# Performance work log

Hardware: AMD Instinct MI355X
Metric: run time of the kernel (lower is better)

## Reference

```python
import jax, jax.numpy as jnp
import numpy as np

N = 500_000
MOL_C = 128
HID_C = 256
NUM_GRAPHS = 16384


def setup_inputs() -> dict:
    key = jax.random.key(0)
    ks = jax.random.split(key, 7)
    fan_lin = (MOL_C + HID_C) ** -0.5
    fan_last = HID_C ** -0.5
    return {
        "input_rep": jax.random.normal(ks[0], (N, MOL_C), dtype=jnp.float32),
        "final_rep": jax.random.normal(ks[1], (N, HID_C), dtype=jnp.float32),
        "graph_index": jnp.sort(jax.random.randint(ks[2], (N,), 0, NUM_GRAPHS, dtype=jnp.int32)),
        "W_lin": jax.random.normal(ks[3], (HID_C, MOL_C + HID_C), dtype=jnp.float32) * fan_lin,
        "b_lin": jax.random.normal(ks[4], (HID_C,), dtype=jnp.float32) * fan_lin,
        "W_last": jax.random.normal(ks[5], (HID_C, HID_C), dtype=jnp.float32) * fan_last,
        "b_last": jax.random.normal(ks[6], (HID_C,), dtype=jnp.float32) * fan_last,
    }


def reference(input_rep, final_rep, graph_index, W_lin, b_lin, W_last, b_last):
    # att = sigmoid(Linear(cat([input_rep, final_rep], dim=1)))  -> [N, HID_C]
    cat = jnp.concatenate([input_rep, final_rep], axis=1)
    att = jax.nn.sigmoid(cat @ W_lin.T + b_lin)
    # gated value: att * Linear(final_rep)  -> [N, HID_C]
    g = att * (final_rep @ W_last.T + b_last)
    # scatter_add over nodes -> [NUM_GRAPHS, HID_C]
    return jax.ops.segment_sum(g, graph_index, num_segments=NUM_GRAPHS)
```

## Files before the change

kernel.cpp:

```cpp
#include <hip/hip_runtime.h>
#include <hip/hip_bf16.h>


#define MOLC 128
#define HIDC 256
#define KTOT 384
#define NKT  12
#define TILE_N 64
#define NTHREADS 256

typedef _Float16 f16;
typedef _Float16 f16x8 __attribute__((ext_vector_type(8)));
typedef float    f32x4 __attribute__((ext_vector_type(4)));

__device__ __host__ __forceinline__ int swz(int r) { return (r ^ (r >> 2)) & 3; }

__device__ __forceinline__ f16x8 cvt8(float4 a, float4 b) {
  f16x8 r;
  r[0] = (f16)a.x; r[1] = (f16)a.y; r[2] = (f16)a.z; r[3] = (f16)a.w;
  r[4] = (f16)b.x; r[5] = (f16)b.y; r[6] = (f16)b.z; r[7] = (f16)b.w;
  return r;
}

#define GLL16(g, l) __builtin_amdgcn_global_load_lds(                          \
    (const __attribute__((address_space(1))) uint32_t*)(g),                    \
    (__attribute__((address_space(3))) uint32_t*)(l), 16, 0, 0)

__global__ void zero_out_kernel(float4* __restrict__ p, int n4) {
  int i = blockIdx.x * blockDim.x + threadIdx.x;
  if (i < n4) p[i] = make_float4(0.f, 0.f, 0.f, 0.f);
}

__global__ void pack_weights_kernel(const float* __restrict__ W_lin,
                                    const float* __restrict__ W_last,
                                    f16* __restrict__ ws) {
  int s = blockIdx.x * blockDim.x + threadIdx.x;
  if (s >= 20480) return;
  const float* src;
  f16* dst;
  if (s < 12288) {
    int ks = s >> 10, r = (s >> 2) & 255, c = s & 3;
    src = W_lin + (size_t)r * KTOT + ks * 32 + ((c ^ swz(r)) * 8);
    dst = ws + (size_t)s * 8;
  } else {
    int s2 = s - 12288;
    int ks = s2 >> 10, r = (s2 >> 2) & 255, c = s2 & 3;
    src = W_last + (size_t)r * HIDC + ks * 32 + ((c ^ swz(r)) * 8);
    dst = ws + 98304 + (size_t)s2 * 8;
  }
  f16x8 v;
#pragma unroll
  for (int j = 0; j < 8; ++j) v[j] = (f16)src[j];
  *(f16x8*)dst = v;
}

__device__ __forceinline__ void stage_w(const f16* gtile, f16* ltile, int wv, int lane) {
#pragma unroll
  for (int c = 0; c < 4; ++c) {
    const int off = (wv * 4 + c) * 1024 + lane * 16;
    GLL16((const char*)gtile + off, (char*)ltile + off);
  }
}

__global__ __launch_bounds__(NTHREADS, 2) void attn_pool_kernel(
    const float* __restrict__ input_rep,
    const float* __restrict__ final_rep,
    const int*   __restrict__ gidx,
    const f16*   __restrict__ ws,
    const float* __restrict__ b_lin,
    const float* __restrict__ b_last,
    float* __restrict__ out,
    int n_nodes)
{
  __shared__ f16 Abuf[2][TILE_N * 32];
  __shared__ f16 W1buf[2][HIDC * 32];
  __shared__ f16 W2buf[2][HIDC * 32];
  __shared__ int gi[TILE_N];

  const int t    = threadIdx.x;
  const int nb   = blockIdx.x * TILE_N;
  const int vn   = min(TILE_N, n_nodes - nb);
  const int lane = t & 63;
  const int wv   = t >> 6;
  const int wch  = wv * 64;
  const int lr   = lane & 15;
  const int lq   = lane >> 4;
  const int sl   = (lq ^ swz(lr)) * 8;

  const int arow  = t >> 2;
  const int aslot = t & 3;
  const int awslot = (aslot ^ swz(arow)) * 8;

  if (t < TILE_N) gi[t] = (nb + t < n_nodes) ? gidx[nb + t] : -1;

  const f16* wsW1 = ws;
  const f16* wsW2 = ws + 98304;

  stage_w(wsW1, W1buf[0], wv, lane);
  {
    float4 x0, x1;
    if (arow < vn) {
      const float* src = input_rep + (size_t)(nb + arow) * MOLC + aslot * 8;
      x0 = ((const float4*)src)[0];
      x1 = ((const float4*)src)[1];
    } else {
      x0 = make_float4(0.f, 0.f, 0.f, 0.f); x1 = x0;
    }
    *(f16x8*)&Abuf[0][arow * 32 + awslot] = cvt8(x0, x1);
  }
  __syncthreads();

  f32x4 acc1[4][4], acc2[4][4];
#pragma unroll
  for (int i = 0; i < 4; ++i)
#pragma unroll
    for (int j = 0; j < 4; ++j) { acc1[i][j] = (f32x4)(0.f); acc2[i][j] = (f32x4)(0.f); }

  for (int ks = 0; ks < NKT; ++ks) {
    const int cur = ks & 1, nxt = cur ^ 1;
    const int kn  = ks + 1;
    const bool pf = (kn < NKT);

    float4 x0, x1;
    if (pf) {
      stage_w(wsW1 + kn * 8192, W1buf[nxt], wv, lane);
      if (kn >= 4) stage_w(wsW2 + (kn - 4) * 8192, W2buf[nxt], wv, lane);
      if (arow < vn) {
        const float* src = (kn < 4)
            ? input_rep + (size_t)(nb + arow) * MOLC + kn * 32 + aslot * 8
            : final_rep + (size_t)(nb + arow) * HIDC + (kn * 32 - MOLC) + aslot * 8;
        x0 = ((const float4*)src)[0];
        x1 = ((const float4*)src)[1];
      } else {
        x0 = make_float4(0.f, 0.f, 0.f, 0.f); x1 = x0;
      }
    }

    f16x8 af[4];
#pragma unroll
    for (int i = 0; i < 4; ++i)
      af[i] = *(const f16x8*)&Abuf[cur][(i * 16 + lr) * 32 + sl];

    {
      f16x8 bf[4];
#pragma unroll
      for (int j = 0; j < 4; ++j)
        bf[j] = *(const f16x8*)&W1buf[cur][(wch + j * 16 + lr) * 32 + sl];
#pragma unroll
      for (int i = 0; i < 4; ++i)
#pragma unroll
        for (int j = 0; j < 4; ++j)
          acc1[i][j] = __builtin_amdgcn_mfma_f32_16x16x32_f16(af[i], bf[j], acc1[i][j], 0, 0, 0);
    }
    if (ks >= 4) {
      f16x8 bf[4];
#pragma unroll
      for (int j = 0; j < 4; ++j)
        bf[j] = *(const f16x8*)&W2buf[cur][(wch + j * 16 + lr) * 32 + sl];
#pragma unroll
      for (int i = 0; i < 4; ++i)
#pragma unroll
        for (int j = 0; j < 4; ++j)
          acc2[i][j] = __builtin_amdgcn_mfma_f32_16x16x32_f16(af[i], bf[j], acc2[i][j], 0, 0, 0);
    }

    if (pf) *(f16x8*)&Abuf[nxt][arow * 32 + awslot] = cvt8(x0, x1);

    __syncthreads();
  }

  float bl[4], bb[4];
#pragma unroll
  for (int j = 0; j < 4; ++j) {
    bl[j] = b_lin[wch + j * 16 + lr];
    bb[j] = b_last[wch + j * 16 + lr];
  }
#pragma unroll
  for (int i = 0; i < 4; ++i)
#pragma unroll
    for (int j = 0; j < 4; ++j)
#pragma unroll
      for (int r = 0; r < 4; ++r) {
        float a   = acc1[i][j][r] + bl[j];
        float att = 1.f / (1.f + __expf(-a));
        acc1[i][j][r] = att * (acc2[i][j][r] + bb[j]);
      }

  for (int i = 0; i < 4; ++i) {
    const int base = i * 16;
    int myg[4];
#pragma unroll
    for (int r = 0; r < 4; ++r) myg[r] = gi[base + lq * 4 + r];

    int s = 0;
    while (s < 16) {
      const int gid = gi[base + s];
      int e = s + 1;
      while (e < 16 && gi[base + e] == gid) ++e;
      if (gid >= 0) {
#pragma unroll
        for (int j = 0; j < 4; ++j) {
          float v = 0.f;
#pragma unroll
          for (int r = 0; r < 4; ++r)
            if (myg[r] == gid) v += acc1[i][j][r];
          v += __shfl_xor(v, 16);
          v += __shfl_xor(v, 32);
          if (lane < 16)
            atomicAdd(&out[(size_t)gid * HIDC + wch + j * 16 + lane], v);
        }
      }
      s = e;
    }
  }
}

extern "C" void kernel_launch(void* const* d_in, const int* in_sizes, int n_in,
                              void* d_out, int out_size, void* d_ws, size_t ws_size,
                              hipStream_t stream) {
  const float* input_rep = (const float*)d_in[0];
  const float* final_rep = (const float*)d_in[1];
  const int*   gidx      = (const int*)d_in[2];
  const float* W_lin     = (const float*)d_in[3];
  const float* b_lin     = (const float*)d_in[4];
  const float* W_last    = (const float*)d_in[5];
  const float* b_last    = (const float*)d_in[6];
  float* out = (float*)d_out;
  f16*   ws  = (f16*)d_ws;

  const int n_nodes = in_sizes[0] / MOLC;

  const int n4 = out_size / 4;
  zero_out_kernel<<<(n4 + 255) / 256, 256, 0, stream>>>((float4*)out, n4);

  pack_weights_kernel<<<80, 256, 0, stream>>>(W_lin, W_last, ws);

  const int grid = (n_nodes + TILE_N - 1) / TILE_N;
  attn_pool_kernel<<<grid, NTHREADS, 0, stream>>>(
      input_rep, final_rep, gidx, ws, b_lin, b_last, out, n_nodes);
}
```

Baseline: 1.022 ms.

## Load activations directly into MFMA registers, double tile with 8 waves, prepack weight fragments

The block tile grows to 128 nodes with 512 threads arranged as 2x4 waves, so each weight tile staged in LDS is reused by twice as many rows. Activation fragments are now loaded straight from global memory into registers in MFMA operand layout and converted to fp16 there, which removes the LDS staging buffer for A. Weights are prepacked in per-lane fragment order so the LDS reads need no swizzle. Synchronisation uses raw s_barrier with explicit vmcnt waits and scheduling barriers in place of __syncthreads. The per-lane activation loads are less coalesced and register pressure goes up.

```diff
diff --git a/kernel.cpp b/kernel.cpp
--- a/kernel.cpp
+++ b/kernel.cpp
@@ -6,14 +6,20 @@
 #define HIDC 256
 #define KTOT 384
 #define NKT  12
-#define TILE_N 64
-#define NTHREADS 256
+#define TILE_N 128
+#define NTH  512
 
 typedef _Float16 f16;
 typedef _Float16 f16x8 __attribute__((ext_vector_type(8)));
 typedef float    f32x4 __attribute__((ext_vector_type(4)));
 
-__device__ __host__ __forceinline__ int swz(int r) { return (r ^ (r >> 2)) & 3; }
+#define SBAR()  __builtin_amdgcn_s_barrier()
+#define SCHED() __builtin_amdgcn_sched_barrier(0)
+#define WAITV8() asm volatile("s_waitcnt vmcnt(8)" ::: "memory")
+
+#define GLL16(g, l) __builtin_amdgcn_global_load_lds(                          \
+    (const __attribute__((address_space(1))) uint32_t*)(g),                    \
+    (__attribute__((address_space(3))) uint32_t*)(l), 16, 0, 0)
 
 __device__ __forceinline__ f16x8 cvt8(float4 a, float4 b) {
   f16x8 r;
@@ -21,10 +27,6 @@
   r[4] = (f16)b.x; r[5] = (f16)b.y; r[6] = (f16)b.z; r[7] = (f16)b.w;
   return r;
 }
-
-#define GLL16(g, l) __builtin_amdgcn_global_load_lds(                          \
-    (const __attribute__((address_space(1))) uint32_t*)(g),                    \
-    (__attribute__((address_space(3))) uint32_t*)(l), 16, 0, 0)
 
 __global__ void zero_out_kernel(float4* __restrict__ p, int n4) {
   int i = blockIdx.x * blockDim.x + threadIdx.x;
@@ -39,30 +41,23 @@
   const float* src;
   f16* dst;
   if (s < 12288) {
-    int ks = s >> 10, r = (s >> 2) & 255, c = s & 3;
-    src = W_lin + (size_t)r * KTOT + ks * 32 + ((c ^ swz(r)) * 8);
+    int ks = s >> 10, rem = s & 1023, g = rem >> 6, lane = rem & 63;
+    int lr = lane & 15, lq = lane >> 4;
+    src = W_lin + (size_t)(g * 16 + lr) * KTOT + ks * 32 + lq * 8;
     dst = ws + (size_t)s * 8;
   } else {
     int s2 = s - 12288;
-    int ks = s2 >> 10, r = (s2 >> 2) & 255, c = s2 & 3;
-    src = W_last + (size_t)r * HIDC + ks * 32 + ((c ^ swz(r)) * 8);
+    int ks = s2 >> 10, rem = s2 & 1023, g = rem >> 6, lane = rem & 63;
+    int lr = lane & 15, lq = lane >> 4;
+    src = W_last + (size_t)(g * 16 + lr) * HIDC + ks * 32 + lq * 8;
     dst = ws + 98304 + (size_t)s2 * 8;
   }
-  f16x8 v;
-#pragma unroll
-  for (int j = 0; j < 8; ++j) v[j] = (f16)src[j];
-  *(f16x8*)dst = v;
-}
-
-__device__ __forceinline__ void stage_w(const f16* gtile, f16* ltile, int wv, int lane) {
-#pragma unroll
-  for (int c = 0; c < 4; ++c) {
-    const int off = (wv * 4 + c) * 1024 + lane * 16;
-    GLL16((const char*)gtile + off, (char*)ltile + off);
-  }
-}
-
-__global__ __launch_bounds__(NTHREADS, 2) void attn_pool_kernel(
+  float4 a = ((const float4*)src)[0];
+  float4 b = ((const float4*)src)[1];
+  *(f16x8*)dst = cvt8(a, b);
+}
+
+__global__ __launch_bounds__(NTH, 2) void attn_pool_kernel(
     const float* __restrict__ input_rep,
     const float* __restrict__ final_rep,
     const int*   __restrict__ gidx,
@@ -72,43 +67,53 @@
     float* __restrict__ out,
     int n_nodes)
 {
-  __shared__ f16 Abuf[2][TILE_N * 32];
-  __shared__ f16 W1buf[2][HIDC * 32];
-  __shared__ f16 W2buf[2][HIDC * 32];
+  __shared__ f16 W[2][16384];
   __shared__ int gi[TILE_N];
 
   const int t    = threadIdx.x;
-  const int nb   = blockIdx.x * TILE_N;
-  const int vn   = min(TILE_N, n_nodes - nb);
   const int lane = t & 63;
   const int wv   = t >> 6;
-  const int wch  = wv * 64;
+  const int wm   = wv >> 2;
+  const int wn   = wv & 3;
   const int lr   = lane & 15;
   const int lq   = lane >> 4;
-  const int sl   = (lq ^ swz(lr)) * 8;
-
-  const int arow  = t >> 2;
-  const int aslot = t & 3;
-  const int awslot = (aslot ^ swz(arow)) * 8;
+  const int nb   = blockIdx.x * TILE_N;
+  const int wch  = wn * 64;
 
   if (t < TILE_N) gi[t] = (nb + t < n_nodes) ? gidx[nb + t] : -1;
 
-  const f16* wsW1 = ws;
-  const f16* wsW2 = ws + 98304;
-
-  stage_w(wsW1, W1buf[0], wv, lane);
-  {
-    float4 x0, x1;
-    if (arow < vn) {
-      const float* src = input_rep + (size_t)(nb + arow) * MOLC + aslot * 8;
-      x0 = ((const float4*)src)[0];
-      x1 = ((const float4*)src)[1];
-    } else {
-      x0 = make_float4(0.f, 0.f, 0.f, 0.f); x1 = x0;
-    }
-    *(f16x8*)&Abuf[0][arow * 32 + awslot] = cvt8(x0, x1);
-  }
-  __syncthreads();
+  int offin[4], offfin[4];
+#pragma unroll
+  for (int i = 0; i < 4; ++i) {
+    int r = nb + wm * 64 + i * 16 + lr;
+    r = min(r, n_nodes - 1);
+    offin[i]  = r * MOLC;
+    offfin[i] = r * HIDC;
+  }
+
+  auto stageW1 = [&](int ks, int b) {
+#pragma unroll
+    for (int rd = 0; rd < 2; ++rd)
+      GLL16(ws + ks * 8192 + rd * 4096 + t * 8, &W[b][rd * 4096 + t * 8]);
+  };
+  auto stageW2 = [&](int ks, int b) {
+#pragma unroll
+    for (int rd = 0; rd < 2; ++rd)
+      GLL16(ws + 98304 + (ks - 4) * 8192 + rd * 4096 + t * 8,
+            &W[b][8192 + rd * 4096 + t * 8]);
+  };
+
+  float4 ra[4][2];
+  auto loadA = [&](int ks) {
+#pragma unroll
+    for (int i = 0; i < 4; ++i) {
+      const float* p = (ks < 4)
+          ? input_rep + offin[i]  + ks * 32 + lq * 8
+          : final_rep + offfin[i] + (ks - 4) * 32 + lq * 8;
+      ra[i][0] = ((const float4*)p)[0];
+      ra[i][1] = ((const float4*)p)[1];
+    }
+  };
 
   f32x4 acc1[4][4], acc2[4][4];
 #pragma unroll
@@ -116,36 +121,38 @@
 #pragma unroll
     for (int j = 0; j < 4; ++j) { acc1[i][j] = (f32x4)(0.f); acc2[i][j] = (f32x4)(0.f); }
 
+  stageW1(0, 0);
+  SCHED();
+  loadA(0);
+  SCHED();
+  asm volatile("s_waitcnt lgkmcnt(0)" ::: "memory");
+  WAITV8();
+  SCHED();
+  SBAR();
+
+#pragma unroll
   for (int ks = 0; ks < NKT; ++ks) {
-    const int cur = ks & 1, nxt = cur ^ 1;
-    const int kn  = ks + 1;
-    const bool pf = (kn < NKT);
-
-    float4 x0, x1;
-    if (pf) {
-      stage_w(wsW1 + kn * 8192, W1buf[nxt], wv, lane);
-      if (kn >= 4) stage_w(wsW2 + (kn - 4) * 8192, W2buf[nxt], wv, lane);
-      if (arow < vn) {
-        const float* src = (kn < 4)
-            ? input_rep + (size_t)(nb + arow) * MOLC + kn * 32 + aslot * 8
-            : final_rep + (size_t)(nb + arow) * HIDC + (kn * 32 - MOLC) + aslot * 8;
-        x0 = ((const float4*)src)[0];
-        x1 = ((const float4*)src)[1];
-      } else {
-        x0 = make_float4(0.f, 0.f, 0.f, 0.f); x1 = x0;
-      }
-    }
+    const int b = ks & 1, nx = b ^ 1;
+
+    if (ks + 1 < NKT) {
+      stageW1(ks + 1, nx);
+      if (ks + 1 >= 4) stageW2(ks + 1, nx);
+    }
+    SCHED();
 
     f16x8 af[4];
 #pragma unroll
-    for (int i = 0; i < 4; ++i)
-      af[i] = *(const f16x8*)&Abuf[cur][(i * 16 + lr) * 32 + sl];
+    for (int i = 0; i < 4; ++i) af[i] = cvt8(ra[i][0], ra[i][1]);
+    SCHED();
+
+    if (ks + 1 < NKT) loadA(ks + 1);
+    SCHED();
 
     {
       f16x8 bf[4];
 #pragma unroll
       for (int j = 0; j < 4; ++j)
-        bf[j] = *(const f16x8*)&W1buf[cur][(wch + j * 16 + lr) * 32 + sl];
+        bf[j] = *(const f16x8*)&W[b][(wn * 4 + j) * 512 + (lq * 16 + lr) * 8];
 #pragma unroll
       for (int i = 0; i < 4; ++i)
 #pragma unroll
@@ -156,7 +163,7 @@
       f16x8 bf[4];
 #pragma unroll
       for (int j = 0; j < 4; ++j)
-        bf[j] = *(const f16x8*)&W2buf[cur][(wch + j * 16 + lr) * 32 + sl];
+        bf[j] = *(const f16x8*)&W[b][8192 + (wn * 4 + j) * 512 + (lq * 16 + lr) * 8];
 #pragma unroll
       for (int i = 0; i < 4; ++i)
 #pragma unroll
@@ -164,9 +171,11 @@
           acc2[i][j] = __builtin_amdgcn_mfma_f32_16x16x32_f16(af[i], bf[j], acc2[i][j], 0, 0, 0);
     }
 
-    if (pf) *(f16x8*)&Abuf[nxt][arow * 32 + awslot] = cvt8(x0, x1);
-
-    __syncthreads();
+    if (ks + 1 < NKT) {
+      WAITV8();
+      SCHED();
+      SBAR();
+    }
   }
 
   float bl[4], bb[4];
@@ -187,7 +196,7 @@
       }
 
   for (int i = 0; i < 4; ++i) {
-    const int base = i * 16;
+    const int base = wm * 64 + i * 16;
     int myg[4];
 #pragma unroll
     for (int r = 0; r < 4; ++r) myg[r] = gi[base + lq * 4 + r];
@@ -236,6 +245,6 @@
   pack_weights_kernel<<<80, 256, 0, stream>>>(W_lin, W_last, ws);
 
   const int grid = (n_nodes + TILE_N - 1) / TILE_N;
-  attn_pool_kernel<<<grid, NTHREADS, 0, stream>>>(
+  attn_pool_kernel<<<grid, NTH, 0, stream>>>(
       input_rep, final_rep, gidx, ws, b_lin, b_last, out, n_nodes);
 }
```

Measured after the change: 1.341 ms. +31.2%, slower.
